# Kernel tuning notes

Measured on AMD Instinct MI355X. Metric: run time of the kernel, lower is better.

## Reference

```python
import jax, jax.numpy as jnp
import numpy as np

B, N, M, D, H = 2, 512, 512, 128, 256
EPS = 1e-5


def _layernorm(x, g, b):
    mu = jnp.mean(x, axis=-1, keepdims=True)
    var = jnp.mean(jnp.square(x - mu), axis=-1, keepdims=True)
    return (x - mu) * jax.lax.rsqrt(var + EPS) * g + b


def setup_inputs() -> dict:
    key = jax.random.key(0)
    ks = jax.random.split(key, 12)
    X = jax.random.normal(ks[0], (B, N, D), dtype=jnp.float32)
    Y = jax.random.normal(ks[1], (B, M, D), dtype=jnp.float32)
    mask = jax.random.randint(ks[2], (B, N, M), 0, 2).astype(jnp.int32)
    s_in = 1.0 / np.sqrt(2 * D)
    s_h = 1.0 / np.sqrt(H)
    s_d = 1.0 / np.sqrt(D)
    # edge-net Linear(2D, H) split into Y-half and X-half (pairs = cat([Y, X]))
    W1y = jax.random.normal(ks[3], (D, H), dtype=jnp.float32) * s_in
    W1x = jax.random.normal(ks[4], (D, H), dtype=jnp.float32) * s_in
    b1 = jnp.zeros((H,), dtype=jnp.float32)
    W2 = jax.random.normal(ks[5], (H, D), dtype=jnp.float32) * s_h
    b2 = jnp.zeros((D,), dtype=jnp.float32)
    Wf1 = jax.random.normal(ks[6], (D, H), dtype=jnp.float32) * s_d
    bf1 = jnp.zeros((H,), dtype=jnp.float32)
    Wf2 = jax.random.normal(ks[7], (H, D), dtype=jnp.float32) * s_h
    bf2 = jnp.zeros((D,), dtype=jnp.float32)
    g0 = jnp.ones((D,), dtype=jnp.float32)
    be0 = jnp.zeros((D,), dtype=jnp.float32)
    g1 = jnp.ones((D,), dtype=jnp.float32)
    be1 = jnp.zeros((D,), dtype=jnp.float32)
    return {"X": X, "Y": Y, "mask": mask, "W1y": W1y, "W1x": W1x, "b1": b1,
            "W2": W2, "b2": b2, "Wf1": Wf1, "bf1": bf1, "Wf2": Wf2, "bf2": bf2,
            "g0": g0, "be0": be0, "g1": g1, "be1": be1}


def reference(X, Y, mask, W1y, W1x, b1, W2, b2, Wf1, bf1, Wf2, bf2, g0, be0, g1, be1):
    # pairs[b,n,m] = concat(Y[b,m], X[b,n]); Linear on concat == sum of two GEMMs,
    # so avoid materializing the [B,N,M,2D] pairs tensor.
    hy = jnp.einsum('bmd,dh->bmh', Y, W1y)          # [B,M,H]
    hx = jnp.einsum('bnd,dh->bnh', X, W1x)          # [B,N,H]
    h = jax.nn.relu(hy[:, None, :, :] + hx[:, :, None, :] + b1)   # [B,N,M,H]
    E = jnp.einsum('bnmh,hd->bnmd', h, W2) + b2     # [B,N,M,D]
    E = E * mask[..., None].astype(E.dtype)         # masked sum-pool over M
    Z = X + jnp.sum(E, axis=2)                      # residual, [B,N,D]
    Z = _layernorm(Z, g0, be0)
    Z = Z + jax.nn.relu(Z @ Wf1 + bf1) @ Wf2 + bf2  # residual MLP
    Z = _layernorm(Z, g1, be1)
    return Z
```

## Files before the change

### kernel.cpp

```cpp
#include <hip/hip_runtime.h>

#define BB 2
#define NN 512
#define MM 512
#define DD 128
#define HH 256

__global__ __launch_bounds__(256) void k_inproj(
    const float* __restrict__ X, const float* __restrict__ Y,
    const float* __restrict__ W1x, const float* __restrict__ W1y,
    const float* __restrict__ b1,
    float* __restrict__ hx, float* __restrict__ hy)
{
    int blk = blockIdx.x, t = threadIdx.x;
    bool isX = blk < 256;
    const float* src = isX ? X : Y;
    const float* W   = isX ? W1x : W1y;
    float* dst       = isX ? hx : hy;
    int row0 = (isX ? blk : blk - 256) * 4;

    const float* r0 = src + (size_t)row0 * DD;
    float bias = isX ? b1[t] : 0.0f;
    float a0 = bias, a1 = bias, a2 = bias, a3 = bias;

#pragma unroll 16
    for (int d = 0; d < DD; ++d) {
        float w = W[(size_t)d * HH + t];
        a0 = fmaf(r0[d         ], w, a0);
        a1 = fmaf(r0[d +   DD  ], w, a1);
        a2 = fmaf(r0[d + 2 * DD], w, a2);
        a3 = fmaf(r0[d + 3 * DD], w, a3);
    }
    dst[(size_t)(row0 + 0) * HH + t] = a0;
    dst[(size_t)(row0 + 1) * HH + t] = a1;
    dst[(size_t)(row0 + 2) * HH + t] = a2;
    dst[(size_t)(row0 + 3) * HH + t] = a3;
}

__global__ __launch_bounds__(512) void k_fused(
    const float* __restrict__ X, const float* __restrict__ hx,
    const float* __restrict__ hy, const int* __restrict__ mask,
    const float* __restrict__ W2, const float* __restrict__ b2,
    const float* __restrict__ Wf1, const float* __restrict__ bf1,
    const float* __restrict__ Wf2, const float* __restrict__ bf2,
    const float* __restrict__ g0, const float* __restrict__ be0,
    const float* __restrict__ g1, const float* __restrict__ be1,
    float* __restrict__ out)
{
    __shared__ float smf[MM][4];
    __shared__ float sSp[2][HH][4];
    __shared__ float sST[HH][4];
    __shared__ float scratch[4][4][DD];
    __shared__ float znT[DD][4];
    __shared__ float sp2[2][HH][4];
    __shared__ float suT[HH][4];
    __shared__ float srow[4][DD];
    __shared__ float scnt[4];

    int blk = blockIdx.x;
    int b = blk >> 7, n0 = (blk & 127) * 4;
    int t = threadIdx.x;
    int wave = t >> 6, lane = t & 63;

    {
        const int* mp = mask + (size_t)(b * NN + n0) * MM + t;
#pragma unroll
        for (int r = 0; r < 4; ++r)
            smf[t][r] = (float)mp[(size_t)r * MM];
    }
    if (wave < 4) {
        const int* mrow = mask + (size_t)(b * NN + n0 + wave) * MM;
        int c = 0;
#pragma unroll
        for (int k = 0; k < 8; ++k) c += mrow[lane + k * 64];
#pragma unroll
        for (int off = 32; off; off >>= 1) c += __shfl_down(c, off);
        if (lane == 0) scnt[wave] = (float)c;
    }
    __syncthreads();

    {
        int h = t & 255, mh = t >> 8;
        float hxv[4];
#pragma unroll
        for (int r = 0; r < 4; ++r)
            hxv[r] = hx[(size_t)(b * NN + n0 + r) * HH + h];
        const float* hyp = hy + ((size_t)b * MM + mh * 256) * HH + h;
        float a0 = 0.f, a1 = 0.f, a2 = 0.f, a3 = 0.f;
#pragma unroll 16
        for (int m = 0; m < 256; ++m) {
            float hyv = hyp[(size_t)m * HH];
            float4 m4 = *(const float4*)&smf[mh * 256 + m][0];
            a0 = fmaf(fmaxf(hxv[0] + hyv, 0.f), m4.x, a0);
            a1 = fmaf(fmaxf(hxv[1] + hyv, 0.f), m4.y, a1);
            a2 = fmaf(fmaxf(hxv[2] + hyv, 0.f), m4.z, a2);
            a3 = fmaf(fmaxf(hxv[3] + hyv, 0.f), m4.w, a3);
        }
        *(float4*)&sSp[mh][h][0] = make_float4(a0, a1, a2, a3);
    }
    __syncthreads();
#pragma unroll
    for (int k = 0; k < 2; ++k) {
        int v = t + k * 512;
        int h = v >> 2, r = v & 3;
        sST[h][r] = sSp[0][h][r] + sSp[1][h][r];
    }
    __syncthreads();

    {
        int d = t & 127, q = t >> 7;
        const float* wp = W2 + (size_t)(q * 64) * DD + d;
        float a0 = 0.f, a1 = 0.f, a2 = 0.f, a3 = 0.f;
#pragma unroll 8
        for (int hh = 0; hh < 64; ++hh) {
            float w = wp[(size_t)hh * DD];
            float4 s4 = *(const float4*)&sST[q * 64 + hh][0];
            a0 = fmaf(s4.x, w, a0); a1 = fmaf(s4.y, w, a1);
            a2 = fmaf(s4.z, w, a2); a3 = fmaf(s4.w, w, a3);
        }
        scratch[q][0][d] = a0; scratch[q][1][d] = a1;
        scratch[q][2][d] = a2; scratch[q][3][d] = a3;
    }
    __syncthreads();
    {
        int r = t >> 7, d = t & 127;
        srow[r][d] = scratch[0][r][d] + scratch[1][r][d]
                   + scratch[2][r][d] + scratch[3][r][d]
                   + X[(size_t)(b * NN + n0 + r) * DD + d] + scnt[r] * b2[d];
    }
    __syncthreads();
    if (wave < 4) {
        float v0 = srow[wave][lane], v1 = srow[wave][lane + 64];
        float s = v0 + v1, q2 = v0 * v0 + v1 * v1;
#pragma unroll
        for (int off = 32; off; off >>= 1) {
            s += __shfl_down(s, off); q2 += __shfl_down(q2, off);
        }
        s = __shfl(s, 0); q2 = __shfl(q2, 0);
        float mu   = s * (1.0f / 128.0f);
        float var  = q2 * (1.0f / 128.0f) - mu * mu;
        float rstd = rsqrtf(var + 1e-5f);
        znT[lane][wave]      = (v0 - mu) * rstd * g0[lane]      + be0[lane];
        znT[lane + 64][wave] = (v1 - mu) * rstd * g0[lane + 64] + be0[lane + 64];
    }
    __syncthreads();

    {
        int h = t & 255, dq = t >> 8;
        float bias = dq ? 0.f : bf1[h];
        float a0 = bias, a1 = bias, a2 = bias, a3 = bias;
        const float* wp = Wf1 + (size_t)(dq * 64) * HH + h;
#pragma unroll 8
        for (int dd = 0; dd < 64; ++dd) {
            float w = wp[(size_t)dd * HH];
            float4 z4 = *(const float4*)&znT[dq * 64 + dd][0];
            a0 = fmaf(z4.x, w, a0); a1 = fmaf(z4.y, w, a1);
            a2 = fmaf(z4.z, w, a2); a3 = fmaf(z4.w, w, a3);
        }
        *(float4*)&sp2[dq][h][0] = make_float4(a0, a1, a2, a3);
    }
    __syncthreads();
#pragma unroll
    for (int k = 0; k < 2; ++k) {
        int v = t + k * 512;
        int h = v >> 2, r = v & 3;
        suT[h][r] = fmaxf(sp2[0][h][r] + sp2[1][h][r], 0.f);
    }
    __syncthreads();

    {
        int d = t & 127, q = t >> 7;
        const float* wp = Wf2 + (size_t)(q * 64) * DD + d;
        float a0 = 0.f, a1 = 0.f, a2 = 0.f, a3 = 0.f;
#pragma unroll 8
        for (int hh = 0; hh < 64; ++hh) {
            float w = wp[(size_t)hh * DD];
            float4 u4 = *(const float4*)&suT[q * 64 + hh][0];
            a0 = fmaf(u4.x, w, a0); a1 = fmaf(u4.y, w, a1);
            a2 = fmaf(u4.z, w, a2); a3 = fmaf(u4.w, w, a3);
        }
        scratch[q][0][d] = a0; scratch[q][1][d] = a1;
        scratch[q][2][d] = a2; scratch[q][3][d] = a3;
    }
    __syncthreads();
    {
        int r = t >> 7, d = t & 127;
        srow[r][d] = znT[d][r] + bf2[d]
                   + scratch[0][r][d] + scratch[1][r][d]
                   + scratch[2][r][d] + scratch[3][r][d];
    }
    __syncthreads();
    if (wave < 4) {
        float v0 = srow[wave][lane], v1 = srow[wave][lane + 64];
        float s = v0 + v1, q2 = v0 * v0 + v1 * v1;
#pragma unroll
        for (int off = 32; off; off >>= 1) {
            s += __shfl_down(s, off); q2 += __shfl_down(q2, off);
        }
        s = __shfl(s, 0); q2 = __shfl(q2, 0);
        float mu   = s * (1.0f / 128.0f);
        float var  = q2 * (1.0f / 128.0f) - mu * mu;
        float rstd = rsqrtf(var + 1e-5f);
        size_t row = (size_t)(b * NN + n0 + wave) * DD;
        out[row + lane]      = (v0 - mu) * rstd * g1[lane]      + be1[lane];
        out[row + lane + 64] = (v1 - mu) * rstd * g1[lane + 64] + be1[lane + 64];
    }
}

extern "C" void kernel_launch(void* const* d_in, const int* in_sizes, int n_in,
                              void* d_out, int out_size, void* d_ws, size_t ws_size,
                              hipStream_t stream)
{
    const float* X    = (const float*)d_in[0];
    const float* Y    = (const float*)d_in[1];
    const int*   mask = (const int*)d_in[2];
    const float* W1y  = (const float*)d_in[3];
    const float* W1x  = (const float*)d_in[4];
    const float* b1   = (const float*)d_in[5];
    const float* W2   = (const float*)d_in[6];
    const float* b2   = (const float*)d_in[7];
    const float* Wf1  = (const float*)d_in[8];
    const float* bf1  = (const float*)d_in[9];
    const float* Wf2  = (const float*)d_in[10];
    const float* bf2  = (const float*)d_in[11];
    const float* g0   = (const float*)d_in[12];
    const float* be0  = (const float*)d_in[13];
    const float* g1   = (const float*)d_in[14];
    const float* be1  = (const float*)d_in[15];
    float* out = (float*)d_out;

    float* ws = (float*)d_ws;
    float* hx = ws;
    float* hy = ws + (size_t)BB * NN * HH;

    k_inproj<<<512, 256, 0, stream>>>(X, Y, W1x, W1y, b1, hx, hy);
    k_fused <<<256, 512, 0, stream>>>(X, hx, hy, mask, W2, b2, Wf1, bf1,
                                      Wf2, bf2, g0, be0, g1, be1, out);
}
```

Measured before the change: 118.4 us.

## Precompute float mask and row counts in inproj; widen fused kernel to 1024 threads

Moves the int-to-float conversion of the mask and the per-row mask counts into the first kernel, which writes them to workspace. The fused kernel now uses 1024 threads per block, splitting the M reduction into four quarters and the inner GEMMs into eight slices, and reads mask values straight from global memory instead of staging them in shared memory. The aim is more parallelism and latency hiding in the dominant pair-reduction loop. In exchange the float mask costs an extra 2 MB workspace round-trip, the reductions gain more shared-memory partial sums, and 1024-thread blocks may reduce occupancy.

```diff
diff --git a/kernel.cpp b/kernel.cpp
--- a/kernel.cpp
+++ b/kernel.cpp
@@ -9,15 +9,35 @@
 __global__ __launch_bounds__(256) void k_inproj(
     const float* __restrict__ X, const float* __restrict__ Y,
     const float* __restrict__ W1x, const float* __restrict__ W1y,
-    const float* __restrict__ b1,
-    float* __restrict__ hx, float* __restrict__ hy)
+    const float* __restrict__ b1, const int* __restrict__ mask,
+    float* __restrict__ hx, float* __restrict__ hy,
+    float* __restrict__ mf, float* __restrict__ cntv)
 {
     int blk = blockIdx.x, t = threadIdx.x;
+
+    {
+        int idx = blk * 256 + t;
+        int4 v = ((const int4*)mask)[idx];
+        ((float4*)mf)[idx] = make_float4((float)v.x, (float)v.y,
+                                         (float)v.z, (float)v.w);
+    }
+
     bool isX = blk < 256;
     const float* src = isX ? X : Y;
     const float* W   = isX ? W1x : W1y;
     float* dst       = isX ? hx : hy;
     int row0 = (isX ? blk : blk - 256) * 4;
+
+    if (isX) {
+        int wave = t >> 6, lane = t & 63;
+        const int* mrow = mask + (size_t)(row0 + wave) * MM;
+        int c = 0;
+#pragma unroll
+        for (int k = 0; k < 8; ++k) c += mrow[lane + k * 64];
+#pragma unroll
+        for (int off = 32; off; off >>= 1) c += __shfl_down(c, off);
+        if (lane == 0) cntv[row0 + wave] = (float)c;
+    }
 
     const float* r0 = src + (size_t)row0 * DD;
     float bias = isX ? b1[t] : 0.0f;
@@ -37,9 +57,10 @@
     dst[(size_t)(row0 + 3) * HH + t] = a3;
 }
 
-__global__ __launch_bounds__(512) void k_fused(
+__global__ __launch_bounds__(1024) void k_fused(
     const float* __restrict__ X, const float* __restrict__ hx,
-    const float* __restrict__ hy, const int* __restrict__ mask,
+    const float* __restrict__ hy, const float* __restrict__ mf,
+    const float* __restrict__ cntv,
     const float* __restrict__ W2, const float* __restrict__ b2,
     const float* __restrict__ Wf1, const float* __restrict__ bf1,
     const float* __restrict__ Wf2, const float* __restrict__ bf2,
@@ -47,89 +68,78 @@
     const float* __restrict__ g1, const float* __restrict__ be1,
     float* __restrict__ out)
 {
-    __shared__ float smf[MM][4];
-    __shared__ float sSp[2][HH][4];
-    __shared__ float sST[HH][4];
-    __shared__ float scratch[4][4][DD];
+    __shared__ float sSp[4][4][HH];
+    __shared__ float sST[4][HH];
+    __shared__ float scratch[8][4][DD];
     __shared__ float znT[DD][4];
-    __shared__ float sp2[2][HH][4];
-    __shared__ float suT[HH][4];
+    __shared__ float sp2[4][4][HH];
+    __shared__ float suT[4][HH];
     __shared__ float srow[4][DD];
-    __shared__ float scnt[4];
-
-    int blk = blockIdx.x;
-    int b = blk >> 7, n0 = (blk & 127) * 4;
+
     int t = threadIdx.x;
-    int wave = t >> 6, lane = t & 63;
-
-    {
-        const int* mp = mask + (size_t)(b * NN + n0) * MM + t;
+    int grow0 = blockIdx.x * 4;
+    int b = grow0 >> 9;
+
+    {
+        int h = t & 255, mq = t >> 8;
+        float hxv[4];
 #pragma unroll
         for (int r = 0; r < 4; ++r)
-            smf[t][r] = (float)mp[(size_t)r * MM];
-    }
-    if (wave < 4) {
-        const int* mrow = mask + (size_t)(b * NN + n0 + wave) * MM;
-        int c = 0;
-#pragma unroll
-        for (int k = 0; k < 8; ++k) c += mrow[lane + k * 64];
-#pragma unroll
-        for (int off = 32; off; off >>= 1) c += __shfl_down(c, off);
-        if (lane == 0) scnt[wave] = (float)c;
-    }
-    __syncthreads();
-
-    {
-        int h = t & 255, mh = t >> 8;
-        float hxv[4];
-#pragma unroll
-        for (int r = 0; r < 4; ++r)
-            hxv[r] = hx[(size_t)(b * NN + n0 + r) * HH + h];
-        const float* hyp = hy + ((size_t)b * MM + mh * 256) * HH + h;
+            hxv[r] = hx[(size_t)(grow0 + r) * HH + h];
+        const float* hyp = hy + ((size_t)(b * MM) + mq * 128) * HH + h;
+        const float* mfp = mf + (size_t)grow0 * MM + mq * 128;
         float a0 = 0.f, a1 = 0.f, a2 = 0.f, a3 = 0.f;
-#pragma unroll 16
-        for (int m = 0; m < 256; ++m) {
+#pragma unroll 8
+        for (int m = 0; m < 128; ++m) {
             float hyv = hyp[(size_t)m * HH];
-            float4 m4 = *(const float4*)&smf[mh * 256 + m][0];
-            a0 = fmaf(fmaxf(hxv[0] + hyv, 0.f), m4.x, a0);
-            a1 = fmaf(fmaxf(hxv[1] + hyv, 0.f), m4.y, a1);
-            a2 = fmaf(fmaxf(hxv[2] + hyv, 0.f), m4.z, a2);
-            a3 = fmaf(fmaxf(hxv[3] + hyv, 0.f), m4.w, a3);
-        }
-        *(float4*)&sSp[mh][h][0] = make_float4(a0, a1, a2, a3);
-    }
-    __syncthreads();
-#pragma unroll
-    for (int k = 0; k < 2; ++k) {
-        int v = t + k * 512;
-        int h = v >> 2, r = v & 3;
-        sST[h][r] = sSp[0][h][r] + sSp[1][h][r];
+            float w0 = mfp[m         ];
+            float w1 = mfp[m +     MM];
+            float w2 = mfp[m + 2 * MM];
+            float w3 = mfp[m + 3 * MM];
+            a0 = fmaf(fmaxf(hxv[0] + hyv, 0.f), w0, a0);
+            a1 = fmaf(fmaxf(hxv[1] + hyv, 0.f), w1, a1);
+            a2 = fmaf(fmaxf(hxv[2] + hyv, 0.f), w2, a2);
+            a3 = fmaf(fmaxf(hxv[3] + hyv, 0.f), w3, a3);
+        }
+        sSp[mq][0][h] = a0; sSp[mq][1][h] = a1;
+        sSp[mq][2][h] = a2; sSp[mq][3][h] = a3;
+    }
+    __syncthreads();
+    {
+        int r = t >> 8, h = t & 255;
+        sST[r][h] = sSp[0][r][h] + sSp[1][r][h] + sSp[2][r][h] + sSp[3][r][h];
     }
     __syncthreads();
 
     {
         int d = t & 127, q = t >> 7;
-        const float* wp = W2 + (size_t)(q * 64) * DD + d;
+        int hb = q * 32;
+        const float* wp = W2 + (size_t)hb * DD + d;
         float a0 = 0.f, a1 = 0.f, a2 = 0.f, a3 = 0.f;
 #pragma unroll 8
-        for (int hh = 0; hh < 64; ++hh) {
+        for (int hh = 0; hh < 32; ++hh) {
             float w = wp[(size_t)hh * DD];
-            float4 s4 = *(const float4*)&sST[q * 64 + hh][0];
-            a0 = fmaf(s4.x, w, a0); a1 = fmaf(s4.y, w, a1);
-            a2 = fmaf(s4.z, w, a2); a3 = fmaf(s4.w, w, a3);
+            a0 = fmaf(sST[0][hb + hh], w, a0);
+            a1 = fmaf(sST[1][hb + hh], w, a1);
+            a2 = fmaf(sST[2][hb + hh], w, a2);
+            a3 = fmaf(sST[3][hb + hh], w, a3);
         }
         scratch[q][0][d] = a0; scratch[q][1][d] = a1;
         scratch[q][2][d] = a2; scratch[q][3][d] = a3;
     }
     __syncthreads();
-    {
+    if (t < 512) {
         int r = t >> 7, d = t & 127;
-        srow[r][d] = scratch[0][r][d] + scratch[1][r][d]
-                   + scratch[2][r][d] + scratch[3][r][d]
-                   + X[(size_t)(b * NN + n0 + r) * DD + d] + scnt[r] * b2[d];
-    }
-    __syncthreads();
-    if (wave < 4) {
+        float s = scratch[0][r][d] + scratch[1][r][d]
+                + scratch[2][r][d] + scratch[3][r][d]
+                + scratch[4][r][d] + scratch[5][r][d]
+                + scratch[6][r][d] + scratch[7][r][d];
+        srow[r][d] = s + X[(size_t)(grow0 + r) * DD + d]
+                   + cntv[grow0 + r] * b2[d];
+    }
+    __syncthreads();
+    if (t < 256) {
+        int wave = t >> 6, lane = t & 63;
         float v0 = srow[wave][lane], v1 = srow[wave][lane + 64];
         float s = v0 + v1, q2 = v0 * v0 + v1 * v1;
 #pragma unroll
@@ -147,50 +157,56 @@
 
     {
         int h = t & 255, dq = t >> 8;
-        float bias = dq ? 0.f : bf1[h];
+        int db = dq * 32;
+        float bias = (dq == 0) ? bf1[h] : 0.f;
         float a0 = bias, a1 = bias, a2 = bias, a3 = bias;
-        const float* wp = Wf1 + (size_t)(dq * 64) * HH + h;
-#pragma unroll 8
-        for (int dd = 0; dd < 64; ++dd) {
+        const float* wp = Wf1 + (size_t)db * HH + h;
+#pragma unroll 8
+        for (int dd = 0; dd < 32; ++dd) {
             float w = wp[(size_t)dd * HH];
-            float4 z4 = *(const float4*)&znT[dq * 64 + dd][0];
+            float4 z4 = *(const float4*)&znT[db + dd][0];
             a0 = fmaf(z4.x, w, a0); a1 = fmaf(z4.y, w, a1);
             a2 = fmaf(z4.z, w, a2); a3 = fmaf(z4.w, w, a3);
         }
-        *(float4*)&sp2[dq][h][0] = make_float4(a0, a1, a2, a3);
-    }
-    __syncthreads();
-#pragma unroll
-    for (int k = 0; k < 2; ++k) {
-        int v = t + k * 512;
-        int h = v >> 2, r = v & 3;
-        suT[h][r] = fmaxf(sp2[0][h][r] + sp2[1][h][r], 0.f);
+        sp2[dq][0][h] = a0; sp2[dq][1][h] = a1;
+        sp2[dq][2][h] = a2; sp2[dq][3][h] = a3;
+    }
+    __syncthreads();
+    {
+        int r = t >> 8, h = t & 255;
+        suT[r][h] = fmaxf(sp2[0][r][h] + sp2[1][r][h]
+                        + sp2[2][r][h] + sp2[3][r][h], 0.f);
     }
     __syncthreads();
 
     {
         int d = t & 127, q = t >> 7;
-        const float* wp = Wf2 + (size_t)(q * 64) * DD + d;
+        int hb = q * 32;
+        const float* wp = Wf2 + (size_t)hb * DD + d;
         float a0 = 0.f, a1 = 0.f, a2 = 0.f, a3 = 0.f;
 #pragma unroll 8
-        for (int hh = 0; hh < 64; ++hh) {
+        for (int hh = 0; hh < 32; ++hh) {
             float w = wp[(size_t)hh * DD];
-            float4 u4 = *(const float4*)&suT[q * 64 + hh][0];
-            a0 = fmaf(u4.x, w, a0); a1 = fmaf(u4.y, w, a1);
-            a2 = fmaf(u4.z, w, a2); a3 = fmaf(u4.w, w, a3);
+            a0 = fmaf(suT[0][hb + hh], w, a0);
+            a1 = fmaf(suT[1][hb + hh], w, a1);
+            a2 = fmaf(suT[2][hb + hh], w, a2);
+            a3 = fmaf(suT[3][hb + hh], w, a3);
         }
         scratch[q][0][d] = a0; scratch[q][1][d] = a1;
         scratch[q][2][d] = a2; scratch[q][3][d] = a3;
     }
     __syncthreads();
-    {
+    if (t < 512) {
         int r = t >> 7, d = t & 127;
-        srow[r][d] = znT[d][r] + bf2[d]
-                   + scratch[0][r][d] + scratch[1][r][d]
-                   + scratch[2][r][d] + scratch[3][r][d];
-    }
-    __syncthreads();
-    if (wave < 4) {
+        float s = scratch[0][r][d] + scratch[1][r][d]
+                + scratch[2][r][d] + scratch[3][r][d]
+                + scratch[4][r][d] + scratch[5][r][d]
+                + scratch[6][r][d] + scratch[7][r][d];
+        srow[r][d] = znT[d][r] + s + bf2[d];
+    }
+    __syncthreads();
+    if (t < 256) {
+        int wave = t >> 6, lane = t & 63;
         float v0 = srow[wave][lane], v1 = srow[wave][lane + 64];
         float s = v0 + v1, q2 = v0 * v0 + v1 * v1;
 #pragma unroll
@@ -201,7 +217,7 @@
         float mu   = s * (1.0f / 128.0f);
         float var  = q2 * (1.0f / 128.0f) - mu * mu;
         float rstd = rsqrtf(var + 1e-5f);
-        size_t row = (size_t)(b * NN + n0 + wave) * DD;
+        size_t row = (size_t)(grow0 + wave) * DD;
         out[row + lane]      = (v0 - mu) * rstd * g1[lane]      + be1[lane];
         out[row + lane + 64] = (v1 - mu) * rstd * g1[lane + 64] + be1[lane + 64];
     }
@@ -229,11 +245,14 @@
     const float* be1  = (const float*)d_in[15];
     float* out = (float*)d_out;
 
-    float* ws = (float*)d_ws;
-    float* hx = ws;
-    float* hy = ws + (size_t)BB * NN * HH;
-
-    k_inproj<<<512, 256, 0, stream>>>(X, Y, W1x, W1y, b1, hx, hy);
-    k_fused <<<256, 512, 0, stream>>>(X, hx, hy, mask, W2, b2, Wf1, bf1,
-                                      Wf2, bf2, g0, be0, g1, be1, out);
+    float* ws   = (float*)d_ws;
+    float* hx   = ws;
+    float* hy   = hx + (size_t)BB * NN * HH;
+    float* mf   = hy + (size_t)BB * MM * HH;
+    float* cntv = mf + (size_t)BB * NN * MM;
+
+    k_inproj<<<512, 256, 0, stream>>>(X, Y, W1x, W1y, b1, mask,
+                                      hx, hy, mf, cntv);
+    k_fused <<<256, 1024, 0, stream>>>(X, hx, hy, mf, cntv, W2, b2, Wf1, bf1,
+                                       Wf2, bf2, g0, be0, g1, be1, out);
 }
```

New measurement: 119.9 us. Within noise of the previous version (+1.3%).
